# Performance work log

Hardware: AMD Instinct MI355X
Metric: run time of the kernel (lower is better)

## Reference

```python
import jax, jax.numpy as jnp
import numpy as np


def _chamfer(x, y):
    # x: [B, N, 3], y: [B, M, 3]
    x2 = jnp.sum(x * x, axis=-1)                      # [B, N]
    y2 = jnp.sum(y * y, axis=-1)                      # [B, M]
    xy = jnp.einsum('bnd,bmd->bnm', x, y)             # [B, N, M]
    d = x2[:, :, None] + y2[:, None, :] - 2.0 * xy    # [B, N, M]
    cham_x = jnp.min(d, axis=2).mean(axis=1)          # nearest y for each x
    cham_y = jnp.min(d, axis=1).mean(axis=1)          # nearest x for each y
    # pytorch3d default: mean over points, mean over batch, sum of both directions
    return jnp.mean(cham_x + cham_y)


def setup_inputs() -> dict:
    key = jax.random.key(0)
    kx, ky = jax.random.split(key)
    B, N, M, D = 4, 8192, 8192, 3
    x = jax.random.normal(kx, (B, N, D), dtype=jnp.float32)
    y = jax.random.normal(ky, (B, M, D), dtype=jnp.float32)
    return {"x": x, "y": y}


def reference(x, y):
    return _chamfer(x, y)
```

## Files before the change

### kernel.cpp

```cpp
#include <hip/hip_runtime.h>


#define BATCH   4
#define NPTS    8192
#define TPB     256
#define CSLICE  512
#define QT      2
#define QBLK    (4 * QT * 32)
#define MT      (CSLICE / 32)
#define SLICES  (NPTS / CSLICE)
#define QBLKS   (NPTS / QBLK)

typedef _Float16 h8   __attribute__((ext_vector_type(8)));
typedef float    f16v __attribute__((ext_vector_type(16)));

__device__ __forceinline__ void split16(float v, _Float16& hi, _Float16& lo) {
    hi = (_Float16)v;
    lo = (_Float16)(v - (float)hi);
}

__device__ __forceinline__ float tree16(const f16v& d) {
    float g0 = fminf(fminf(d[0],  d[1]),  d[2]);
    float g1 = fminf(fminf(d[3],  d[4]),  d[5]);
    float g2 = fminf(fminf(d[6],  d[7]),  d[8]);
    float g3 = fminf(fminf(d[9],  d[10]), d[11]);
    float g4 = fminf(fminf(d[12], d[13]), d[14]);
    float h0 = fminf(fminf(g0, g1), d[15]);
    float h1 = fminf(fminf(g2, g3), g4);
    return fminf(h0, h1);
}

__global__ __launch_bounds__(TPB, 8) void chamfer_mfma(const float* __restrict__ xg,
                                                       const float* __restrict__ yg,
                                                       float* __restrict__ partial,
                                                       float* __restrict__ out) {
    __shared__ h8 afrag[CSLICE * 2];

    const int tid    = threadIdx.x;
    const int qblock = blockIdx.x;
    const int slice  = blockIdx.y & (SLICES - 1);
    const int b      = blockIdx.y >> 4;
    const int dir    = blockIdx.z;
    const int lane   = tid & 63, wave = tid >> 6;
    const int col    = lane & 31, hv = lane >> 5;

    if (tid == 0) out[0] = 0.0f;
    const float* q = dir ? yg : xg;
    const float* r = dir ? xg : yg;

    const float* rbase = r + ((size_t)b * NPTS + slice * CSLICE) * 3;
#pragma unroll
    for (int i = 0; i < CSLICE / TPB; ++i) {
        const int p = tid + i * TPB;
        float r0 = rbase[p * 3 + 0], r1 = rbase[p * 3 + 1], r2 = rbase[p * 3 + 2];
        _Float16 h0, l0, h1, l1, h2, l2, rnh, rnl;
        split16(r0, h0, l0);
        split16(r1, h1, l1);
        split16(r2, h2, l2);
        split16(fmaf(r0, r0, fmaf(r1, r1, r2 * r2)), rnh, rnl);
        const int base = (p >> 5) * 64 + (p & 31);
        afrag[base]      = (h8){h0, h1, h2, l0, l1, l2, h0, h1};
        afrag[base + 32] = (h8){h2, rnh, rnl, (_Float16)1.0f, (_Float16)1.0f,
                                (_Float16)0.0f, (_Float16)0.0f, (_Float16)0.0f};
    }

    h8 bq[QT];
#pragma unroll
    for (int t = 0; t < QT; ++t) {
        const int qi = qblock * QBLK + (wave * QT + t) * 32 + col;
        const float* qp = q + ((size_t)b * NPTS + qi) * 3;
        float x0 = qp[0], x1 = qp[1], x2 = qp[2];
        _Float16 H0, L0, H1, L1, H2, L2, qnh, qnl;
        split16(-2.0f * x0, H0, L0);
        split16(-2.0f * x1, H1, L1);
        split16(-2.0f * x2, H2, L2);
        split16(fmaf(x0, x0, fmaf(x1, x1, x2 * x2)), qnh, qnl);
        h8 b0 = {H0, H1, H2, H0, H1, H2, L0, L1};
        h8 b1 = {L2, (_Float16)1.0f, (_Float16)1.0f, qnh, qnl,
                 (_Float16)0.0f, (_Float16)0.0f, (_Float16)0.0f};
        bq[t] = hv ? b1 : b0;
    }
    __syncthreads();

    float cm[QT];
#pragma unroll
    for (int t = 0; t < QT; ++t) cm[t] = 3.0e38f;

    for (int mt = 0; mt < MT; ++mt) {
        const h8 ar = afrag[mt * 64 + lane];
        f16v d0, d1;
        asm("v_mfma_f32_32x32x16_f16 %0, %2, %3, 0\n\t"
            "v_mfma_f32_32x32x16_f16 %1, %2, %4, 0\n\t"
            "s_nop 7\n\t"
            "s_nop 7"
            : "=v"(d0), "=v"(d1)
            : "v"(ar), "v"(bq[0]), "v"(bq[1]));
        cm[0] = fminf(cm[0], tree16(d0));
        cm[1] = fminf(cm[1], tree16(d1));
    }

    float* pp = partial + ((size_t)(dir * BATCH + b) * SLICES + slice) * NPTS
                        + qblock * QBLK;
#pragma unroll
    for (int t = 0; t < QT; ++t) {
        cm[t] = fminf(cm[t], __shfl_xor(cm[t], 32, 64));
        if (hv == 0)
            pp[(wave * QT + t) * 32 + col] = cm[t];
    }
}

__global__ __launch_bounds__(TPB) void chamfer_reduce(const float* __restrict__ partial,
                                                      float* __restrict__ out) {
    const int tid = threadIdx.x;
    const int g   = blockIdx.x * TPB + tid;
    const int db  = g >> 13;
    const int n   = g & (NPTS - 1);

    const float* p = partial + (size_t)db * SLICES * NPTS + n;
    float v = 3.0e38f;
#pragma unroll
    for (int s = 0; s < SLICES; ++s)
        v = fminf(v, p[(size_t)s * NPTS]);

    float w = v;
#pragma unroll
    for (int off = 32; off > 0; off >>= 1)
        w += __shfl_down(w, off, 64);
    __shared__ float ss[TPB / 64];
    if ((tid & 63) == 0) ss[tid >> 6] = w;
    __syncthreads();
    if (tid == 0)
        atomicAdd(out, (ss[0] + ss[1] + ss[2] + ss[3]) * (1.0f / (float)(BATCH * NPTS)));
}

extern "C" void kernel_launch(void* const* d_in, const int* in_sizes, int n_in,
                              void* d_out, int out_size, void* d_ws, size_t ws_size,
                              hipStream_t stream) {
    const float* x = (const float*)d_in[0];
    const float* y = (const float*)d_in[1];
    float* out = (float*)d_out;
    float* partial = (float*)d_ws;

    chamfer_mfma<<<dim3(QBLKS, BATCH * SLICES, 2), TPB, 0, stream>>>(x, y, partial, out);
    chamfer_reduce<<<dim3(2 * BATCH * NPTS / TPB), TPB, 0, stream>>>(partial, out);
}
```

Measured before the change: 80.06 us.

## Fuse chamfer min and reduce into single kernel with double-buffered reference chunks

Replaces the slice-split MFMA kernel plus separate reduce kernel with one kernel. Each block now owns 64 queries and streams the whole reference set through double-buffered LDS chunks, with the four waves splitting the reference tiles. Per-wave minima are combined in shared memory and atomically summed into the output. This removes the partial-buffer round trip and the second launch, but it cuts the grid to 1024 blocks with a long serial loop and adds a __syncthreads per chunk.

Measured after the change: 83.03 us. 1.04x slower.

```diff
diff --git a/kernel.cpp b/kernel.cpp
--- a/kernel.cpp
+++ b/kernel.cpp
@@ -4,12 +4,11 @@
 #define BATCH   4
 #define NPTS    8192
 #define TPB     256
-#define CSLICE  512
-#define QT      2
-#define QBLK    (4 * QT * 32)
-#define MT      (CSLICE / 32)
-#define SLICES  (NPTS / CSLICE)
+#define CHUNK   512
+#define NCHUNK  (NPTS / CHUNK)
+#define QBLK    64
 #define QBLKS   (NPTS / QBLK)
+#define TPW     4
 
 typedef _Float16 h8   __attribute__((ext_vector_type(8)));
 typedef float    f16v __attribute__((ext_vector_type(16)));
@@ -30,44 +29,27 @@
     return fminf(h0, h1);
 }
 
-__global__ __launch_bounds__(TPB, 8) void chamfer_mfma(const float* __restrict__ xg,
+__global__ __launch_bounds__(TPB, 4) void chamfer_mono(const float* __restrict__ xg,
                                                        const float* __restrict__ yg,
-                                                       float* __restrict__ partial,
                                                        float* __restrict__ out) {
-    __shared__ h8 afrag[CSLICE * 2];
+    __shared__ h8    afrag[2][CHUNK * 2];
+    __shared__ float scm[4][2][32];
 
     const int tid    = threadIdx.x;
     const int qblock = blockIdx.x;
-    const int slice  = blockIdx.y & (SLICES - 1);
-    const int b      = blockIdx.y >> 4;
+    const int b      = blockIdx.y;
     const int dir    = blockIdx.z;
     const int lane   = tid & 63, wave = tid >> 6;
     const int col    = lane & 31, hv = lane >> 5;
 
-    if (tid == 0) out[0] = 0.0f;
     const float* q = dir ? yg : xg;
     const float* r = dir ? xg : yg;
+    const float* rbase = r + (size_t)b * NPTS * 3;
 
-    const float* rbase = r + ((size_t)b * NPTS + slice * CSLICE) * 3;
+    h8 bq[2];
 #pragma unroll
-    for (int i = 0; i < CSLICE / TPB; ++i) {
-        const int p = tid + i * TPB;
-        float r0 = rbase[p * 3 + 0], r1 = rbase[p * 3 + 1], r2 = rbase[p * 3 + 2];
-        _Float16 h0, l0, h1, l1, h2, l2, rnh, rnl;
-        split16(r0, h0, l0);
-        split16(r1, h1, l1);
-        split16(r2, h2, l2);
-        split16(fmaf(r0, r0, fmaf(r1, r1, r2 * r2)), rnh, rnl);
-        const int base = (p >> 5) * 64 + (p & 31);
-        afrag[base]      = (h8){h0, h1, h2, l0, l1, l2, h0, h1};
-        afrag[base + 32] = (h8){h2, rnh, rnl, (_Float16)1.0f, (_Float16)1.0f,
-                                (_Float16)0.0f, (_Float16)0.0f, (_Float16)0.0f};
-    }
-
-    h8 bq[QT];
-#pragma unroll
-    for (int t = 0; t < QT; ++t) {
-        const int qi = qblock * QBLK + (wave * QT + t) * 32 + col;
+    for (int t = 0; t < 2; ++t) {
+        const int qi = qblock * QBLK + t * 32 + col;
         const float* qp = q + ((size_t)b * NPTS + qi) * 3;
         float x0 = qp[0], x1 = qp[1], x2 = qp[2];
         _Float16 H0, L0, H1, L1, H2, L2, qnh, qnl;
@@ -80,57 +62,95 @@
                  (_Float16)0.0f, (_Float16)0.0f, (_Float16)0.0f};
         bq[t] = hv ? b1 : b0;
     }
+
+#pragma unroll
+    for (int i = 0; i < CHUNK / TPB; ++i) {
+        const int p = tid + i * TPB;
+        const float* s = rbase + (size_t)p * 3;
+        float r0 = s[0], r1 = s[1], r2 = s[2];
+        _Float16 h0, l0, h1, l1, h2, l2, rnh, rnl;
+        split16(r0, h0, l0);
+        split16(r1, h1, l1);
+        split16(r2, h2, l2);
+        split16(fmaf(r0, r0, fmaf(r1, r1, r2 * r2)), rnh, rnl);
+        const int base = (p >> 5) * 64 + (p & 31);
+        afrag[0][base]      = (h8){h0, h1, h2, l0, l1, l2, h0, h1};
+        afrag[0][base + 32] = (h8){h2, rnh, rnl, (_Float16)1.0f, (_Float16)1.0f,
+                                   (_Float16)0.0f, (_Float16)0.0f, (_Float16)0.0f};
+    }
     __syncthreads();
 
-    float cm[QT];
+    float cm[2] = {3.0e38f, 3.0e38f};
+
+    for (int c = 0; c < NCHUNK; ++c) {
+        const int cur = c & 1;
+
+        float pc[CHUNK / TPB][3];
+        if (c + 1 < NCHUNK) {
 #pragma unroll
-    for (int t = 0; t < QT; ++t) cm[t] = 3.0e38f;
+            for (int i = 0; i < CHUNK / TPB; ++i) {
+                const int p = tid + i * TPB;
+                const float* s = rbase + ((size_t)(c + 1) * CHUNK + p) * 3;
+                pc[i][0] = s[0]; pc[i][1] = s[1]; pc[i][2] = s[2];
+            }
+        }
 
-    for (int mt = 0; mt < MT; ++mt) {
-        const h8 ar = afrag[mt * 64 + lane];
-        f16v d0, d1;
-        asm("v_mfma_f32_32x32x16_f16 %0, %2, %3, 0\n\t"
-            "v_mfma_f32_32x32x16_f16 %1, %2, %4, 0\n\t"
-            "s_nop 7\n\t"
-            "s_nop 7"
-            : "=v"(d0), "=v"(d1)
-            : "v"(ar), "v"(bq[0]), "v"(bq[1]));
-        cm[0] = fminf(cm[0], tree16(d0));
-        cm[1] = fminf(cm[1], tree16(d1));
+#pragma unroll
+        for (int pr = 0; pr < 2; ++pr) {
+            const int rt = wave * TPW + pr * 2;
+            const h8 ar0 = afrag[cur][rt * 64 + lane];
+            const h8 ar1 = afrag[cur][rt * 64 + 64 + lane];
+            f16v d0, d1, d2, d3;
+            asm("v_mfma_f32_32x32x16_f16 %0, %4, %6, 0\n\t"
+                "v_mfma_f32_32x32x16_f16 %1, %4, %7, 0\n\t"
+                "v_mfma_f32_32x32x16_f16 %2, %5, %6, 0\n\t"
+                "v_mfma_f32_32x32x16_f16 %3, %5, %7, 0\n\t"
+                "s_nop 7\n\t"
+                "s_nop 7"
+                : "=&v"(d0), "=&v"(d1), "=&v"(d2), "=&v"(d3)
+                : "v"(ar0), "v"(ar1), "v"(bq[0]), "v"(bq[1]));
+            cm[0] = fminf(cm[0], tree16(d0));
+            cm[1] = fminf(cm[1], tree16(d1));
+            cm[0] = fminf(cm[0], tree16(d2));
+            cm[1] = fminf(cm[1], tree16(d3));
+        }
+
+        if (c + 1 < NCHUNK) {
+#pragma unroll
+            for (int i = 0; i < CHUNK / TPB; ++i) {
+                const int p = tid + i * TPB;
+                float r0 = pc[i][0], r1 = pc[i][1], r2 = pc[i][2];
+                _Float16 h0, l0, h1, l1, h2, l2, rnh, rnl;
+                split16(r0, h0, l0);
+                split16(r1, h1, l1);
+                split16(r2, h2, l2);
+                split16(fmaf(r0, r0, fmaf(r1, r1, r2 * r2)), rnh, rnl);
+                const int base = (p >> 5) * 64 + (p & 31);
+                afrag[cur ^ 1][base]      = (h8){h0, h1, h2, l0, l1, l2, h0, h1};
+                afrag[cur ^ 1][base + 32] = (h8){h2, rnh, rnl, (_Float16)1.0f,
+                                                 (_Float16)1.0f, (_Float16)0.0f,
+                                                 (_Float16)0.0f, (_Float16)0.0f};
+            }
+        }
+        __syncthreads();
     }
 
-    float* pp = partial + ((size_t)(dir * BATCH + b) * SLICES + slice) * NPTS
-                        + qblock * QBLK;
 #pragma unroll
-    for (int t = 0; t < QT; ++t) {
+    for (int t = 0; t < 2; ++t) {
         cm[t] = fminf(cm[t], __shfl_xor(cm[t], 32, 64));
-        if (hv == 0)
-            pp[(wave * QT + t) * 32 + col] = cm[t];
+        if (hv == 0) scm[wave][t][col] = cm[t];
     }
-}
-
-__global__ __launch_bounds__(TPB) void chamfer_reduce(const float* __restrict__ partial,
-                                                      float* __restrict__ out) {
-    const int tid = threadIdx.x;
-    const int g   = blockIdx.x * TPB + tid;
-    const int db  = g >> 13;
-    const int n   = g & (NPTS - 1);
-
-    const float* p = partial + (size_t)db * SLICES * NPTS + n;
-    float v = 3.0e38f;
+    __syncthreads();
+    if (tid < 64) {
+        const int t = tid >> 5, cc = tid & 31;
+        float v = fminf(fminf(scm[0][t][cc], scm[1][t][cc]),
+                        fminf(scm[2][t][cc], scm[3][t][cc]));
 #pragma unroll
-    for (int s = 0; s < SLICES; ++s)
-        v = fminf(v, p[(size_t)s * NPTS]);
-
-    float w = v;
-#pragma unroll
-    for (int off = 32; off > 0; off >>= 1)
-        w += __shfl_down(w, off, 64);
-    __shared__ float ss[TPB / 64];
-    if ((tid & 63) == 0) ss[tid >> 6] = w;
-    __syncthreads();
-    if (tid == 0)
-        atomicAdd(out, (ss[0] + ss[1] + ss[2] + ss[3]) * (1.0f / (float)(BATCH * NPTS)));
+        for (int off = 32; off > 0; off >>= 1)
+            v += __shfl_down(v, off, 64);
+        if (tid == 0)
+            atomicAdd(out, v * (1.0f / (float)(BATCH * NPTS)));
+    }
 }
 
 extern "C" void kernel_launch(void* const* d_in, const int* in_sizes, int n_in,
@@ -139,8 +159,8 @@
     const float* x = (const float*)d_in[0];
     const float* y = (const float*)d_in[1];
     float* out = (float*)d_out;
-    float* partial = (float*)d_ws;
+    (void)d_ws; (void)ws_size;
 
-    chamfer_mfma<<<dim3(QBLKS, BATCH * SLICES, 2), TPB, 0, stream>>>(x, y, partial, out);
-    chamfer_reduce<<<dim3(2 * BATCH * NPTS / TPB), TPB, 0, stream>>>(partial, out);
+    hipMemsetAsync(out, 0, sizeof(float), stream);
+    chamfer_mono<<<dim3(QBLKS, BATCH, 2), TPB, 0, stream>>>(x, y, out);
 }
```
